# Performance work log

Measured on AMD Instinct MI355X. Metric: run time of the kernel, lower is better.

Reference implementation:

```python
import jax, jax.numpy as jnp
import numpy as np
from jax import lax

B, S, DIMS, T, K = 4, 4096, 2048, 10, 2


def setup_inputs() -> dict:
    key = jax.random.key(0)
    ks = jax.random.split(key, 4)
    scale = 1.0 / np.sqrt(DIMS)
    x = jax.random.normal(ks[0], (B, S, DIMS), dtype=jnp.float32)
    W_cls = jax.random.normal(ks[1], (DIMS, T), dtype=jnp.float32) * scale
    W_sparse = jax.random.normal(ks[2], (DIMS, T), dtype=jnp.float32) * scale
    W_gates = jax.random.normal(ks[3], (DIMS, T), dtype=jnp.float32) * scale
    return {
        "x": x,
        "W_cls": W_cls, "b_cls": jnp.zeros((T,), jnp.float32),
        "W_sparse": W_sparse, "b_sparse": jnp.zeros((T,), jnp.float32),
        "W_gates": W_gates, "b_gates": jnp.zeros((T,), jnp.float32),
        "alpha": jnp.ones((1,), jnp.float32),
    }


def reference(x, W_cls, b_cls, W_sparse, b_sparse, W_gates, b_gates, alpha):
    # soft routing: softmax classifier over num_types
    soft_types = jax.nn.softmax(jnp.einsum("bsd,dt->bst", x, W_cls) + b_cls, axis=-1)
    # sparse routing: top-k over logits, softmax over the k kept logits,
    # scattered back into a dense [B,S,T] gate vector (zeros elsewhere)
    logits = jnp.einsum("bsd,dt->bst", x, W_sparse) + b_sparse
    top_v, top_i = lax.top_k(logits, K)                      # [B,S,K]
    sparse_g = jax.nn.softmax(top_v, axis=-1)                # [B,S,K]
    # scatter via one-hot (K and T are tiny)
    sparse_types = jnp.sum(jax.nn.one_hot(top_i, T, dtype=x.dtype) * sparse_g[..., None], axis=-2)  # [B,S,T]
    # per-type sigmoid gates: batched single matmul == stack of Linear(dims,1)+Sigmoid
    gates = jax.nn.sigmoid(jnp.einsum("bsd,dt->bst", x, W_gates) + b_gates)  # [B,S,T]
    a = jax.nn.sigmoid(alpha)                                # [1], broadcasts
    mixed_types = a * sparse_types + (1.0 - a) * soft_types  # [B,S,T]
    # original: gates stacked as [B,S,1,T], mixed unsqueezed to [B,S,1,T], sum over T -> [B,S,1]
    return jnp.sum(gates * mixed_types, axis=-1, keepdims=True)
```

## Files before the change

kernel.cpp:

```cpp
#include <hip/hip_runtime.h>
#include <math.h>
#include <stdint.h>


#define NROWS   16384
#define DIMS_   2048
#define TT      10

typedef __attribute__((ext_vector_type(8))) short short8;
typedef __attribute__((ext_vector_type(4))) float f32x4;

__device__ __forceinline__ unsigned short bf16_rne(float f) {
    unsigned int u = __float_as_uint(f);
    unsigned int r = u + 0x7fffu + ((u >> 16) & 1u);
    return (unsigned short)(r >> 16);
}

__global__ __launch_bounds__(256)
void tgate_k0(const float* __restrict__ W_cls,
              const float* __restrict__ W_sparse,
              const float* __restrict__ W_gates,
              unsigned short* __restrict__ frag)
{
    int t = blockIdx.x * 256 + threadIdx.x;
    int K0   = t >> 7;
    int nt   = (t >> 6) & 1;
    int lane = t & 63;
    int n  = nt * 16 + (lane & 15);
    int kb = K0 * 32 + (lane >> 4) * 8;
    short8 hi, lo;
    #pragma unroll
    for (int j = 0; j < 8; ++j) {
        int k = kb + j;
        float w = 0.0f;
        if (n < 10)      w = W_cls[k * TT + n];
        else if (n < 20) w = W_sparse[k * TT + n - 10];
        else if (n < 30) w = W_gates[k * TT + n - 20];
        unsigned short h = bf16_rne(w);
        float back = __uint_as_float(((unsigned int)h) << 16);
        hi[j] = (short)h;
        lo[j] = (short)bf16_rne(w - back);
    }
    short8* fv = reinterpret_cast<short8*>(frag);
    fv[(K0 * 4 + nt * 2 + 0) * 64 + lane] = hi;
    fv[(K0 * 4 + nt * 2 + 1) * 64 + lane] = lo;
}

__device__ __forceinline__ void issue_chunk(const float* __restrict__ x,
                                            float* bufbase, int row0, int lane,
                                            int colf0)
{
    #pragma unroll
    for (int t = 0; t < 4; ++t) {
        const float* gp = x + (size_t)(row0 + 4 * t + (lane >> 4)) * DIMS_
                            + colf0 + (lane & 15) * 4;
        __builtin_amdgcn_global_load_lds(
            (const __attribute__((address_space(1))) void*)gp,
            (__attribute__((address_space(3))) void*)(bufbase + t * 260),
            16, 0, 0);
    }
}

__global__ __launch_bounds__(1024, 4)
void tgate_k1(const float* __restrict__ x,
              const unsigned short* __restrict__ frag,
              const float* __restrict__ b_cls,
              const float* __restrict__ b_sparse,
              const float* __restrict__ b_gates,
              const float* __restrict__ alpha,
              float* __restrict__ out)
{
    __shared__ alignas(16) float smem[16 * 2080];

    const int tid   = threadIdx.x;
    const int lane  = tid & 63;
    const int wv    = __builtin_amdgcn_readfirstlane(tid >> 6);
    const int row0  = blockIdx.x * 16;
    const int m     = lane & 15;
    const int quad  = lane >> 4;
    const int cbase = wv * 128;

    float* bufs = smem + wv * 2080;
    const short8* fv    = reinterpret_cast<const short8*>(frag);
    const short8* fbase = fv + (4 * wv * 4) * 64 + lane;

    f32x4 accA = (f32x4){0.f, 0.f, 0.f, 0.f};
    f32x4 accB = (f32x4){0.f, 0.f, 0.f, 0.f};

    short8 F[4][4];
    #pragma unroll
    for (int p = 0; p < 4; ++p) {
        #pragma unroll
        for (int j = 0; j < 4; ++j)
            F[p][j] = fbase[(p * 4 + j) * 64];
    }
    __builtin_amdgcn_sched_barrier(0);
    issue_chunk(x, bufs,        row0, lane, cbase);
    issue_chunk(x, bufs + 1040, row0, lane, cbase + 64);
    __builtin_amdgcn_sched_barrier(0);

    __builtin_amdgcn_s_waitcnt(0x0F74);
    __builtin_amdgcn_sched_barrier(0);

    #pragma unroll
    for (int c = 0; c < 2; ++c) {
        if (c == 1) {
            __builtin_amdgcn_s_waitcnt(0x0F70);
            __builtin_amdgcn_sched_barrier(0);
        }
        const float* Lbuf = bufs + c * 1040;
        #pragma unroll
        for (int u = 0; u < 2; ++u) {
            const int p = 2 * c + u;
            const float* src = Lbuf + (m >> 2) * 260 + (m & 3) * 64
                                    + u * 32 + quad * 8;
            float4 b0 = *reinterpret_cast<const float4*>(src);
            float4 b1 = *reinterpret_cast<const float4*>(src + 4);
            float f[8] = {b0.x, b0.y, b0.z, b0.w, b1.x, b1.y, b1.z, b1.w};
            short8 ah, al;
            #pragma unroll
            for (int j = 0; j < 8; ++j) {
                unsigned short hh = bf16_rne(f[j]);
                float back = __uint_as_float(((unsigned int)hh) << 16);
                ah[j] = (short)hh;
                al[j] = (short)bf16_rne(f[j] - back);
            }
            short8 h0 = F[p][0], l0 = F[p][1], h1 = F[p][2], l1 = F[p][3];

            accA = __builtin_amdgcn_mfma_f32_16x16x32_bf16(ah, h0, accA, 0, 0, 0);
            accA = __builtin_amdgcn_mfma_f32_16x16x32_bf16(al, h0, accA, 0, 0, 0);
            accA = __builtin_amdgcn_mfma_f32_16x16x32_bf16(ah, l0, accA, 0, 0, 0);
            accB = __builtin_amdgcn_mfma_f32_16x16x32_bf16(ah, h1, accB, 0, 0, 0);
            accB = __builtin_amdgcn_mfma_f32_16x16x32_bf16(al, h1, accB, 0, 0, 0);
            accB = __builtin_amdgcn_mfma_f32_16x16x32_bf16(ah, l1, accB, 0, 0, 0);
        }
    }

    float* red = smem;
    __syncthreads();
    #pragma unroll
    for (int r = 0; r < 4; ++r) {
        int row = quad * 4 + r;
        red[(wv * 16 + row) * 33 + m]      = accA[r];
        red[(wv * 16 + row) * 33 + m + 16] = accB[r];
    }
    __syncthreads();

    float* fold = red + 16 * 16 * 33;
    if (tid < 256) {
        #pragma unroll
        for (int u = 0; u < 2; ++u) {
            int i = tid * 2 + u;
            int row = i >> 5, j = i & 31;
            float a = 0.0f;
            #pragma unroll
            for (int s = 0; s < 16; ++s) a += red[(s * 16 + row) * 33 + j];
            fold[row * 33 + j] = a;
        }
    }
    __syncthreads();

    if (tid < 16) {
        const float* l = &fold[tid * 33];
        float lc[TT], lsp[TT], g[TT];
        #pragma unroll
        for (int t = 0; t < TT; ++t) {
            lc[t]  = l[t]      + b_cls[t];
            lsp[t] = l[10 + t] + b_sparse[t];
            float lg = l[20 + t] + b_gates[t];
            g[t] = 1.0f / (1.0f + __expf(-lg));
        }
        float mm = lc[0];
        #pragma unroll
        for (int t = 1; t < TT; ++t) mm = fmaxf(mm, lc[t]);
        float esum = 0.0f, gdot = 0.0f;
        #pragma unroll
        for (int t = 0; t < TT; ++t) {
            float e = __expf(lc[t] - mm);
            esum += e;
            gdot = fmaf(g[t], e, gdot);
        }
        float v1 = lsp[0], v2 = -1e30f, gv1 = g[0], gv2 = 0.0f;
        #pragma unroll
        for (int t = 1; t < TT; ++t) {
            if (lsp[t] > v1)      { v2 = v1; gv2 = gv1; v1 = lsp[t]; gv1 = g[t]; }
            else if (lsp[t] > v2) { v2 = lsp[t]; gv2 = g[t]; }
        }
        float s1 = 1.0f / (1.0f + __expf(v2 - v1));
        float s2 = 1.0f - s1;
        float a  = 1.0f / (1.0f + __expf(-alpha[0]));
        float sparse_dot = fmaf(gv1, s1, gv2 * s2);
        out[row0 + tid] = fmaf(a, sparse_dot, (1.0f - a) * (gdot / esum));
    }
}

extern "C" void kernel_launch(void* const* d_in, const int* in_sizes, int n_in,
                              void* d_out, int out_size, void* d_ws, size_t ws_size,
                              hipStream_t stream) {
    const float* x        = (const float*)d_in[0];
    const float* W_cls    = (const float*)d_in[1];
    const float* b_cls    = (const float*)d_in[2];
    const float* W_sparse = (const float*)d_in[3];
    const float* b_sparse = (const float*)d_in[4];
    const float* W_gates  = (const float*)d_in[5];
    const float* b_gates  = (const float*)d_in[6];
    const float* alpha    = (const float*)d_in[7];
    float* out = (float*)d_out;

    unsigned short* frag = (unsigned short*)d_ws;

    tgate_k0<<<dim3(32), dim3(256), 0, stream>>>(W_cls, W_sparse, W_gates, frag);
    tgate_k1<<<dim3(NROWS / 16), dim3(1024), 0, stream>>>(x, frag, b_cls, b_sparse,
                                                          b_gates, alpha, out);
}
```

Measured before the change: 212.8 us.

## Process four row tiles per block with register-pipelined direct global loads

```diff
diff --git a/kernel.cpp b/kernel.cpp
--- a/kernel.cpp
+++ b/kernel.cpp
@@ -6,6 +6,7 @@
 #define NROWS   16384
 #define DIMS_   2048
 #define TT      10
+#define TPB     4
 
 typedef __attribute__((ext_vector_type(8))) short short8;
 typedef __attribute__((ext_vector_type(4))) float f32x4;
@@ -46,21 +47,6 @@
     fv[(K0 * 4 + nt * 2 + 1) * 64 + lane] = lo;
 }
 
-__device__ __forceinline__ void issue_chunk(const float* __restrict__ x,
-                                            float* bufbase, int row0, int lane,
-                                            int colf0)
-{
-    #pragma unroll
-    for (int t = 0; t < 4; ++t) {
-        const float* gp = x + (size_t)(row0 + 4 * t + (lane >> 4)) * DIMS_
-                            + colf0 + (lane & 15) * 4;
-        __builtin_amdgcn_global_load_lds(
-            (const __attribute__((address_space(1))) void*)gp,
-            (__attribute__((address_space(3))) void*)(bufbase + t * 260),
-            16, 0, 0);
-    }
-}
-
 __global__ __launch_bounds__(1024, 4)
 void tgate_k1(const float* __restrict__ x,
               const unsigned short* __restrict__ frag,
@@ -70,22 +56,17 @@
               const float* __restrict__ alpha,
               float* __restrict__ out)
 {
-    __shared__ alignas(16) float smem[16 * 2080];
+    __shared__ alignas(16) float red_lds[16 * 16 * 33 + 16 * 33];
 
     const int tid   = threadIdx.x;
     const int lane  = tid & 63;
     const int wv    = __builtin_amdgcn_readfirstlane(tid >> 6);
-    const int row0  = blockIdx.x * 16;
     const int m     = lane & 15;
     const int quad  = lane >> 4;
-    const int cbase = wv * 128;
-
-    float* bufs = smem + wv * 2080;
+    const int t0    = blockIdx.x * TPB;
+
     const short8* fv    = reinterpret_cast<const short8*>(frag);
     const short8* fbase = fv + (4 * wv * 4) * 64 + lane;
-
-    f32x4 accA = (f32x4){0.f, 0.f, 0.f, 0.f};
-    f32x4 accB = (f32x4){0.f, 0.f, 0.f, 0.f};
 
     short8 F[4][4];
     #pragma unroll
@@ -95,103 +76,121 @@
             F[p][j] = fbase[(p * 4 + j) * 64];
     }
     __builtin_amdgcn_sched_barrier(0);
-    issue_chunk(x, bufs,        row0, lane, cbase);
-    issue_chunk(x, bufs + 1040, row0, lane, cbase + 64);
+
+    float4 xa[3], xb[3];
+    #define ISSUE(g)                                                          \
+    {                                                                         \
+        const int tt_ = (g) >> 2, pp_ = (g) & 3;                              \
+        const float* sp_ = x + (size_t)((t0 + tt_) * 16 + m) * DIMS_          \
+                             + wv * 128 + pp_ * 32 + quad * 8;                \
+        xa[(g) % 3] = *reinterpret_cast<const float4*>(sp_);                  \
+        xb[(g) % 3] = *reinterpret_cast<const float4*>(sp_ + 4);              \
+    }
+    ISSUE(0)
+    ISSUE(1)
     __builtin_amdgcn_sched_barrier(0);
 
-    __builtin_amdgcn_s_waitcnt(0x0F74);
-    __builtin_amdgcn_sched_barrier(0);
+    f32x4 accA = (f32x4){0.f, 0.f, 0.f, 0.f};
+    f32x4 accB = (f32x4){0.f, 0.f, 0.f, 0.f};
+
+    float* red  = red_lds;
+    float* fold = red_lds + 16 * 16 * 33;
 
     #pragma unroll
-    for (int c = 0; c < 2; ++c) {
-        if (c == 1) {
-            __builtin_amdgcn_s_waitcnt(0x0F70);
+    for (int g = 0; g < 16; ++g) {
+        if (g + 2 < 16) { ISSUE(g + 2) }
+        __builtin_amdgcn_sched_barrier(0);
+        if (g < 14)       __builtin_amdgcn_s_waitcnt(0x0F74);
+        else if (g == 14) __builtin_amdgcn_s_waitcnt(0x0F72);
+        else              __builtin_amdgcn_s_waitcnt(0x0F70);
+        __builtin_amdgcn_sched_barrier(0);
+
+        const int p = g & 3;
+        float4 b0 = xa[g % 3];
+        float4 b1 = xb[g % 3];
+        float f[8] = {b0.x, b0.y, b0.z, b0.w, b1.x, b1.y, b1.z, b1.w};
+        short8 ah, al;
+        #pragma unroll
+        for (int j = 0; j < 8; ++j) {
+            unsigned short hh = bf16_rne(f[j]);
+            float back = __uint_as_float(((unsigned int)hh) << 16);
+            ah[j] = (short)hh;
+            al[j] = (short)bf16_rne(f[j] - back);
+        }
+        short8 h0 = F[p][0], l0 = F[p][1], h1 = F[p][2], l1 = F[p][3];
+
+        accA = __builtin_amdgcn_mfma_f32_16x16x32_bf16(ah, h0, accA, 0, 0, 0);
+        accA = __builtin_amdgcn_mfma_f32_16x16x32_bf16(al, h0, accA, 0, 0, 0);
+        accA = __builtin_amdgcn_mfma_f32_16x16x32_bf16(ah, l0, accA, 0, 0, 0);
+        accB = __builtin_amdgcn_mfma_f32_16x16x32_bf16(ah, h1, accB, 0, 0, 0);
+        accB = __builtin_amdgcn_mfma_f32_16x16x32_bf16(al, h1, accB, 0, 0, 0);
+        accB = __builtin_amdgcn_mfma_f32_16x16x32_bf16(ah, l1, accB, 0, 0, 0);
+
+        if (p == 3) {
+            const int tile = t0 + (g >> 2);
+            #pragma unroll
+            for (int r = 0; r < 4; ++r) {
+                int row = quad * 4 + r;
+                red[(wv * 16 + row) * 33 + m]      = accA[r];
+                red[(wv * 16 + row) * 33 + m + 16] = accB[r];
+            }
+            __builtin_amdgcn_s_waitcnt(0xC07F);
             __builtin_amdgcn_sched_barrier(0);
+            __builtin_amdgcn_s_barrier();
+
+            if (tid < 256) {
+                #pragma unroll
+                for (int u = 0; u < 2; ++u) {
+                    int i = tid * 2 + u;
+                    int row = i >> 5, j = i & 31;
+                    float a = 0.0f;
+                    #pragma unroll
+                    for (int s = 0; s < 16; ++s) a += red[(s * 16 + row) * 33 + j];
+                    fold[row * 33 + j] = a;
+                }
+            }
+            __builtin_amdgcn_s_waitcnt(0xC07F);
+            __builtin_amdgcn_sched_barrier(0);
+            __builtin_amdgcn_s_barrier();
+
+            if (tid < 16) {
+                const float* l = &fold[tid * 33];
+                float lc[TT], lsp[TT], gg[TT];
+                #pragma unroll
+                for (int t = 0; t < TT; ++t) {
+                    lc[t]  = l[t]      + b_cls[t];
+                    lsp[t] = l[10 + t] + b_sparse[t];
+                    float lg = l[20 + t] + b_gates[t];
+                    gg[t] = 1.0f / (1.0f + __expf(-lg));
+                }
+                float mm = lc[0];
+                #pragma unroll
+                for (int t = 1; t < TT; ++t) mm = fmaxf(mm, lc[t]);
+                float esum = 0.0f, gdot = 0.0f;
+                #pragma unroll
+                for (int t = 0; t < TT; ++t) {
+                    float e = __expf(lc[t] - mm);
+                    esum += e;
+                    gdot = fmaf(gg[t], e, gdot);
+                }
+                float v1 = lsp[0], v2 = -1e30f, gv1 = gg[0], gv2 = 0.0f;
+                #pragma unroll
+                for (int t = 1; t < TT; ++t) {
+                    if (lsp[t] > v1)      { v2 = v1; gv2 = gv1; v1 = lsp[t]; gv1 = gg[t]; }
+                    else if (lsp[t] > v2) { v2 = lsp[t]; gv2 = gg[t]; }
+                }
+                float s1 = 1.0f / (1.0f + __expf(v2 - v1));
+                float s2 = 1.0f - s1;
+                float a  = 1.0f / (1.0f + __expf(-alpha[0]));
+                float sparse_dot = fmaf(gv1, s1, gv2 * s2);
+                out[tile * 16 + tid] = fmaf(a, sparse_dot, (1.0f - a) * (gdot / esum));
+            }
+
+            accA = (f32x4){0.f, 0.f, 0.f, 0.f};
+            accB = (f32x4){0.f, 0.f, 0.f, 0.f};
         }
-        const float* Lbuf = bufs + c * 1040;
-        #pragma unroll
-        for (int u = 0; u < 2; ++u) {
-            const int p = 2 * c + u;
-            const float* src = Lbuf + (m >> 2) * 260 + (m & 3) * 64
-                                    + u * 32 + quad * 8;
-            float4 b0 = *reinterpret_cast<const float4*>(src);
-            float4 b1 = *reinterpret_cast<const float4*>(src + 4);
-            float f[8] = {b0.x, b0.y, b0.z, b0.w, b1.x, b1.y, b1.z, b1.w};
-            short8 ah, al;
-            #pragma unroll
-            for (int j = 0; j < 8; ++j) {
-                unsigned short hh = bf16_rne(f[j]);
-                float back = __uint_as_float(((unsigned int)hh) << 16);
-                ah[j] = (short)hh;
-                al[j] = (short)bf16_rne(f[j] - back);
-            }
-            short8 h0 = F[p][0], l0 = F[p][1], h1 = F[p][2], l1 = F[p][3];
-
-            accA = __builtin_amdgcn_mfma_f32_16x16x32_bf16(ah, h0, accA, 0, 0, 0);
-            accA = __builtin_amdgcn_mfma_f32_16x16x32_bf16(al, h0, accA, 0, 0, 0);
-            accA = __builtin_amdgcn_mfma_f32_16x16x32_bf16(ah, l0, accA, 0, 0, 0);
-            accB = __builtin_amdgcn_mfma_f32_16x16x32_bf16(ah, h1, accB, 0, 0, 0);
-            accB = __builtin_amdgcn_mfma_f32_16x16x32_bf16(al, h1, accB, 0, 0, 0);
-            accB = __builtin_amdgcn_mfma_f32_16x16x32_bf16(ah, l1, accB, 0, 0, 0);
-        }
-    }
-
-    float* red = smem;
-    __syncthreads();
-    #pragma unroll
-    for (int r = 0; r < 4; ++r) {
-        int row = quad * 4 + r;
-        red[(wv * 16 + row) * 33 + m]      = accA[r];
-        red[(wv * 16 + row) * 33 + m + 16] = accB[r];
-    }
-    __syncthreads();
-
-    float* fold = red + 16 * 16 * 33;
-    if (tid < 256) {
-        #pragma unroll
-        for (int u = 0; u < 2; ++u) {
-            int i = tid * 2 + u;
-            int row = i >> 5, j = i & 31;
-            float a = 0.0f;
-            #pragma unroll
-            for (int s = 0; s < 16; ++s) a += red[(s * 16 + row) * 33 + j];
-            fold[row * 33 + j] = a;
-        }
-    }
-    __syncthreads();
-
-    if (tid < 16) {
-        const float* l = &fold[tid * 33];
-        float lc[TT], lsp[TT], g[TT];
-        #pragma unroll
-        for (int t = 0; t < TT; ++t) {
-            lc[t]  = l[t]      + b_cls[t];
-            lsp[t] = l[10 + t] + b_sparse[t];
-            float lg = l[20 + t] + b_gates[t];
-            g[t] = 1.0f / (1.0f + __expf(-lg));
-        }
-        float mm = lc[0];
-        #pragma unroll
-        for (int t = 1; t < TT; ++t) mm = fmaxf(mm, lc[t]);
-        float esum = 0.0f, gdot = 0.0f;
-        #pragma unroll
-        for (int t = 0; t < TT; ++t) {
-            float e = __expf(lc[t] - mm);
-            esum += e;
-            gdot = fmaf(g[t], e, gdot);
-        }
-        float v1 = lsp[0], v2 = -1e30f, gv1 = g[0], gv2 = 0.0f;
-        #pragma unroll
-        for (int t = 1; t < TT; ++t) {
-            if (lsp[t] > v1)      { v2 = v1; gv2 = gv1; v1 = lsp[t]; gv1 = g[t]; }
-            else if (lsp[t] > v2) { v2 = lsp[t]; gv2 = g[t]; }
-        }
-        float s1 = 1.0f / (1.0f + __expf(v2 - v1));
-        float s2 = 1.0f - s1;
-        float a  = 1.0f / (1.0f + __expf(-alpha[0]));
-        float sparse_dot = fmaf(gv1, s1, gv2 * s2);
-        out[row0 + tid] = fmaf(a, sparse_dot, (1.0f - a) * (gdot / esum));
-    }
+    }
+    #undef ISSUE
 }
 
 extern "C" void kernel_launch(void* const* d_in, const int* in_sizes, int n_in,
@@ -210,6 +209,6 @@
     unsigned short* frag = (unsigned short*)d_ws;
 
     tgate_k0<<<dim3(32), dim3(256), 0, stream>>>(W_cls, W_sparse, W_gates, frag);
-    tgate_k1<<<dim3(NROWS / 16), dim3(1024), 0, stream>>>(x, frag, b_cls, b_sparse,
-                                                          b_gates, alpha, out);
-}
+    tgate_k1<<<dim3(NROWS / 16 / TPB), dim3(1024), 0, stream>>>(
+        x, frag, b_cls, b_sparse, b_gates, alpha, out);
+}
```

New measurement: 207.3 us. 2.6% less time.
